# Performance work log

Hardware: AMD Instinct MI355X
Metric: run time of the kernel (lower is better)

## Reference

```python
import jax, jax.numpy as jnp
import numpy as np

N_NODES = 50000
N_EDGES = 800000
N_GRAPHS = 64
D_IN = 768
D_HID = 256


def gcn_conv(x, src, dst, W, b, n_nodes):
    """PyG GCNConv: symmetric-normalized aggregation with self-loops.
    out = D^{-1/2} (A + I) D^{-1/2} (x @ W) + b
    """
    h = x @ W  # [N, C_out]
    # degree from target nodes, counting the implicit self-loop (+1)
    deg = jax.ops.segment_sum(jnp.ones((src.shape[0],), h.dtype), dst,
                              num_segments=n_nodes) + 1.0
    dinv = jax.lax.rsqrt(deg)  # deg >= 1 always (self-loop)
    norm = (dinv[src] * dinv[dst])[:, None]  # [E, 1]
    agg = jax.ops.segment_sum(h[src] * norm, dst, num_segments=n_nodes)
    # self-loop contribution: norm_ii = dinv_i^2
    agg = agg + (dinv * dinv)[:, None] * h
    return agg + b


def global_mean_pool(x, batch, n_graphs):
    s = jax.ops.segment_sum(x, batch, num_segments=n_graphs)
    cnt = jax.ops.segment_sum(jnp.ones((x.shape[0],), x.dtype), batch,
                              num_segments=n_graphs)
    return s / jnp.maximum(cnt, 1.0)[:, None]


def setup_inputs() -> dict:
    key = jax.random.key(0)
    ks = jax.random.split(key, 12)
    x = jax.random.normal(ks[0], (N_NODES, D_IN), jnp.float32)
    edge_index = jax.random.randint(ks[1], (2, N_EDGES), 0, N_NODES, jnp.int64)
    batch = jnp.sort(jax.random.randint(ks[2], (N_NODES,), 0, N_GRAPHS, jnp.int64))
    def glorot(k, shape):
        lim = np.sqrt(6.0 / (shape[0] + shape[1]))
        return jax.random.uniform(k, shape, jnp.float32, -lim, lim)
    return {
        "x": x, "edge_index": edge_index, "batch": batch,
        "W1": glorot(ks[3], (D_IN, D_HID)), "b1": jnp.zeros((D_HID,), jnp.float32),
        "W2": glorot(ks[4], (D_HID, D_HID)), "b2": jnp.zeros((D_HID,), jnp.float32),
        "W3": glorot(ks[5], (D_HID, D_HID)), "b3": jnp.zeros((D_HID,), jnp.float32),
        "Wl": glorot(ks[6], (D_HID, D_IN)), "bl": jnp.zeros((D_IN,), jnp.float32),
    }


def reference(x, edge_index, batch, W1, b1, W2, b2, W3, b3, Wl, bl):
    src, dst = edge_index[0], edge_index[1]
    n = x.shape[0]
    # dropout is identity in eval mode
    h = jax.nn.relu(gcn_conv(x, src, dst, W1, b1, n))
    h = jax.nn.relu(gcn_conv(h, src, dst, W2, b2, n))
    h = gcn_conv(h, src, dst, W3, b3, n)
    g = global_mean_pool(h, batch, N_GRAPHS)  # [G, D_HID]
    return g @ Wl + bl  # [G, D_IN]
```

## Files before the change

kernel.cpp:

```cpp
#include <hip/hip_runtime.h>
#include <hip/hip_bf16.h>

#define D_IN 768
#define D_HID 256

typedef __attribute__((ext_vector_type(8))) short short8;
typedef __attribute__((ext_vector_type(4))) float f32x4;

__device__ inline float b2f(unsigned short u) {
    unsigned x = ((unsigned)u) << 16;
    union { unsigned u; float f; } c; c.u = x; return c.f;
}
__device__ inline unsigned short f2b(float v) {
    __hip_bfloat16 h = __float2bfloat16(v);
    return *(unsigned short*)&h;
}

__device__ inline void gload_lds16(const void* g, void* l) {
    __builtin_amdgcn_global_load_lds(
        (const __attribute__((address_space(1))) unsigned int*)g,
        (__attribute__((address_space(3))) unsigned int*)l, 16, 0, 0);
}


__global__ void k_count(const int* __restrict__ dst, int* __restrict__ deg, int E) {
    int i = blockIdx.x * 256 + threadIdx.x;
    if (i < E) atomicAdd(&deg[dst[i]], 1);
}

__global__ void k_dinv(const int* __restrict__ deg, float* __restrict__ dinv, int N) {
    int i = blockIdx.x * 256 + threadIdx.x;
    if (i < N) dinv[i] = rsqrtf((float)deg[i] + 1.0f);
}

__global__ __launch_bounds__(1024) void k_scan(const int* __restrict__ deg,
                                               int* __restrict__ row_ptr, int N) {
    __shared__ int wsum[16];
    __shared__ int carry_s;
    int t = threadIdx.x;
    int lane = t & 63, wid = t >> 6;
    if (t == 0) carry_s = 0;
    __syncthreads();
    for (int base = 0; base < N; base += 1024) {
        int i = base + t;
        int v = (i < N) ? deg[i] : 0;
        int s = v;
        #pragma unroll
        for (int d = 1; d < 64; d <<= 1) {
            int tmp = __shfl_up(s, d);
            if (lane >= d) s += tmp;
        }
        if (lane == 63) wsum[wid] = s;
        __syncthreads();
        if (wid == 0 && lane < 16) {
            int ws = wsum[lane];
            #pragma unroll
            for (int d = 1; d < 16; d <<= 1) {
                int tmp = __shfl_up(ws, d);
                if (lane >= d) ws += tmp;
            }
            wsum[lane] = ws;
        }
        __syncthreads();
        int carry = carry_s;
        int woff = (wid > 0) ? wsum[wid - 1] : 0;
        if (i < N) row_ptr[i] = carry + woff + s - v;
        __syncthreads();
        if (t == 0) carry_s = carry + wsum[15];
        __syncthreads();
    }
    if (t == 0) row_ptr[N] = carry_s;
}

__global__ void k_fill(const int* __restrict__ src, const int* __restrict__ dst,
                       const int* __restrict__ row_ptr, int* __restrict__ wptr,
                       int* __restrict__ csr_src, int E) {
    int i = blockIdx.x * 256 + threadIdx.x;
    if (i < E) {
        int d = dst[i];
        int w = atomicAdd(&wptr[d], 1);
        csr_src[row_ptr[d] + w] = src[i];
    }
}

__global__ void k_bounds(const int* __restrict__ batch, int* __restrict__ cnt,
                         int* __restrict__ offg, int N, int G) {
    int g = threadIdx.x;
    if (g >= G) return;
    auto lower = [&](int key) {
        int lo = 0, hi = N;
        while (lo < hi) {
            int mid = (lo + hi) >> 1;
            if (batch[mid] < key) lo = mid + 1; else hi = mid;
        }
        return lo;
    };
    int lo = lower(g);
    int hi = lower(g + 1);
    offg[g] = lo;
    cnt[g] = hi - lo;
}

__global__ void k_prep_B(const float* __restrict__ W, short* __restrict__ Bp, int KA) {
    int t = blockIdx.x * 256 + threadIdx.x;
    if (t >= KA * 256) return;
    int k = t >> 8, n = t & 255;
    float v = W[(size_t)k * 256 + n];
    unsigned short h = f2b(v);
    unsigned short l = f2b(v - b2f(h));
    int c = k >> 5, q = (k >> 3) & 3, j = k & 7;
    int tile = n >> 4, ln = n & 15;
    size_t base = (size_t)c * 16384 + (size_t)(tile * 4 + q) * 128 + ln * 8 + j;
    Bp[base] = (short)h;
    Bp[base + 8192] = (short)l;
}

template <int MODE>
__global__ __launch_bounds__(256, 2) void k_gemm4(const void* __restrict__ Av,
                                                  const short* __restrict__ Bp,
                                                  unsigned short* __restrict__ C,
                                                  int M) {
    constexpr int KA = (MODE == 1) ? D_IN : D_HID;
    constexpr int NCH = KA / 32;
    __shared__ short Bs[2][16384];

    int t = threadIdx.x;
    int lane = t & 63, w = t >> 6;
    int ln = lane & 15, q = lane >> 4;
    int bm = blockIdx.x * 64;

    const char* Abase[4];
    #pragma unroll
    for (int s = 0; s < 4; ++s) {
        int rr = bm + s * 16 + ln;
        rr = (rr < M) ? rr : (M - 1);
        Abase[s] = (const char*)Av + (size_t)rr * KA * ((MODE == 1) ? 4 : 2);
    }

    f32x4 acc[4][4];
    #pragma unroll
    for (int s = 0; s < 4; ++s)
        #pragma unroll
        for (int tt = 0; tt < 4; ++tt) acc[s][tt] = (f32x4){0.f, 0.f, 0.f, 0.f};

    auto stage = [&](int c, int pb) {
        #pragma unroll
        for (int i = 0; i < 8; ++i) {
            int seg = i * 4 + w;
            gload_lds16(Bp + (size_t)c * 16384 + seg * 512 + lane * 8,
                        &Bs[pb][seg * 512]);
        }
    };

    stage(0, 0);
    __syncthreads();

    for (int c = 0; c < NCH; ++c) {
        int pb = c & 1;
        if (c + 1 < NCH) stage(c + 1, pb ^ 1);

        short8 a_hi[4], a_lo[4];
        #pragma unroll
        for (int s = 0; s < 4; ++s) {
            if (MODE == 1) {
                const float* Af = (const float*)(Abase[s]) + c * 32 + q * 8;
                f32x4 v0 = *(const f32x4*)Af;
                f32x4 v1 = *(const f32x4*)(Af + 4);
                float vv[8] = {v0[0], v0[1], v0[2], v0[3], v1[0], v1[1], v1[2], v1[3]};
                #pragma unroll
                for (int j = 0; j < 8; ++j) {
                    unsigned short h = f2b(vv[j]);
                    a_hi[s][j] = (short)h;
                    a_lo[s][j] = (short)f2b(vv[j] - b2f(h));
                }
            } else {
                const unsigned short* Ab = (const unsigned short*)(Abase[s]) + c * 32 + q * 8;
                a_hi[s] = *(const short8*)Ab;
            }
        }

        #pragma unroll
        for (int tt = 0; tt < 4; ++tt) {
            int T = w * 4 + tt;
            const short* bp = &Bs[pb][(size_t)(T * 4 + q) * 128 + ln * 8];
            short8 bh = *(const short8*)bp;
            short8 bl = *(const short8*)(bp + 8192);
            #pragma unroll
            for (int s = 0; s < 4; ++s) {
                acc[s][tt] = __builtin_amdgcn_mfma_f32_16x16x32_bf16(a_hi[s], bh, acc[s][tt], 0, 0, 0);
                if (MODE == 1)
                    acc[s][tt] = __builtin_amdgcn_mfma_f32_16x16x32_bf16(a_lo[s], bh, acc[s][tt], 0, 0, 0);
                acc[s][tt] = __builtin_amdgcn_mfma_f32_16x16x32_bf16(
                    (MODE == 1) ? a_hi[s] : a_hi[s], bl, acc[s][tt], 0, 0, 0);
            }
        }
        __syncthreads();
    }

    #pragma unroll
    for (int s = 0; s < 4; ++s)
        #pragma unroll
        for (int tt = 0; tt < 4; ++tt)
            #pragma unroll
            for (int r = 0; r < 4; ++r) {
                int row = bm + s * 16 + q * 4 + r;
                if (row < M)
                    C[(size_t)row * 256 + w * 64 + tt * 16 + ln] = f2b(acc[s][tt][r]);
            }
}

template <int RELU, int OUTBF>
__global__ __launch_bounds__(256) void k_agg(const unsigned short* __restrict__ hin,
                                             void* __restrict__ hout,
                                             const int* __restrict__ row_ptr,
                                             const int* __restrict__ csr_src,
                                             const float* __restrict__ dinv,
                                             const float* __restrict__ bias, int N) {
    int w = threadIdx.x >> 6;
    int lane = threadIdx.x & 63;
    int row = blockIdx.x * 4 + w;
    if (row >= N) return;
    int c4 = lane * 4;
    int s = row_ptr[row], e = row_ptr[row + 1];
    float a0 = 0.f, a1 = 0.f, a2 = 0.f, a3 = 0.f;
    int j = s;
    for (; j + 4 <= e; j += 4) {
        int u0 = csr_src[j], u1 = csr_src[j + 1], u2 = csr_src[j + 2], u3 = csr_src[j + 3];
        float d0 = dinv[u0], d1 = dinv[u1], d2 = dinv[u2], d3 = dinv[u3];
        ushort4 v0 = *(const ushort4*)&hin[(size_t)u0 * 256 + c4];
        ushort4 v1 = *(const ushort4*)&hin[(size_t)u1 * 256 + c4];
        ushort4 v2 = *(const ushort4*)&hin[(size_t)u2 * 256 + c4];
        ushort4 v3 = *(const ushort4*)&hin[(size_t)u3 * 256 + c4];
        a0 += d0 * b2f(v0.x) + d1 * b2f(v1.x) + d2 * b2f(v2.x) + d3 * b2f(v3.x);
        a1 += d0 * b2f(v0.y) + d1 * b2f(v1.y) + d2 * b2f(v2.y) + d3 * b2f(v3.y);
        a2 += d0 * b2f(v0.z) + d1 * b2f(v1.z) + d2 * b2f(v2.z) + d3 * b2f(v3.z);
        a3 += d0 * b2f(v0.w) + d1 * b2f(v1.w) + d2 * b2f(v2.w) + d3 * b2f(v3.w);
    }
    for (; j < e; ++j) {
        int u = csr_src[j];
        float d = dinv[u];
        ushort4 v = *(const ushort4*)&hin[(size_t)u * 256 + c4];
        a0 += d * b2f(v.x); a1 += d * b2f(v.y); a2 += d * b2f(v.z); a3 += d * b2f(v.w);
    }
    float di = dinv[row];
    float dii = di * di;
    ushort4 vs = *(const ushort4*)&hin[(size_t)row * 256 + c4];
    float4 bb = *(const float4*)&bias[c4];
    a0 = a0 * di + dii * b2f(vs.x) + bb.x;
    a1 = a1 * di + dii * b2f(vs.y) + bb.y;
    a2 = a2 * di + dii * b2f(vs.z) + bb.z;
    a3 = a3 * di + dii * b2f(vs.w) + bb.w;
    if (RELU) {
        a0 = fmaxf(a0, 0.f); a1 = fmaxf(a1, 0.f);
        a2 = fmaxf(a2, 0.f); a3 = fmaxf(a3, 0.f);
    }
    if (OUTBF) {
        ushort4 o; o.x = f2b(a0); o.y = f2b(a1); o.z = f2b(a2); o.w = f2b(a3);
        *(ushort4*)((unsigned short*)hout + (size_t)row * 256 + c4) = o;
    } else {
        *(float4*)((float*)hout + (size_t)row * 256 + c4) = make_float4(a0, a1, a2, a3);
    }
}

__global__ __launch_bounds__(256) void k_pool(const float* __restrict__ h,
                                              const int* __restrict__ cnt,
                                              const int* __restrict__ offg,
                                              float* __restrict__ g) {
    int gi = blockIdx.x, slice = blockIdx.y;
    int c = threadIdx.x;
    int start = offg[gi], n = cnt[gi];
    int per = (n + (int)gridDim.y - 1) / (int)gridDim.y;
    int r0 = slice * per;
    int r1 = min(n, r0 + per);
    float acc = 0.f;
    for (int r = r0; r < r1; ++r) acc += h[(size_t)(start + r) * D_HID + c];
    if (r1 > r0) atomicAdd(&g[gi * D_HID + c], acc);
}

__global__ __launch_bounds__(256) void k_final(const float* __restrict__ g,
                                               const int* __restrict__ cnt,
                                               const float* __restrict__ Wl,
                                               const float* __restrict__ bl,
                                               float* __restrict__ out) {
    __shared__ float gs[D_HID];
    int t = threadIdx.x;
    int gi = blockIdx.y;
    int c = blockIdx.x * 256 + t;
    float inv = 1.0f / (float)max(cnt[gi], 1);
    gs[t] = g[gi * D_HID + t] * inv;
    __syncthreads();
    float acc = bl[c];
    #pragma unroll 8
    for (int k = 0; k < D_HID; ++k) acc = fmaf(gs[k], Wl[(size_t)k * D_IN + c], acc);
    out[(size_t)gi * D_IN + c] = acc;
}


extern "C" void kernel_launch(void* const* d_in, const int* in_sizes, int n_in,
                              void* d_out, int out_size, void* d_ws, size_t ws_size,
                              hipStream_t stream) {
    const float* x     = (const float*)d_in[0];
    const int*   ei    = (const int*)d_in[1];
    const int*   batch = (const int*)d_in[2];
    const float* W1 = (const float*)d_in[3];
    const float* b1 = (const float*)d_in[4];
    const float* W2 = (const float*)d_in[5];
    const float* b2 = (const float*)d_in[6];
    const float* W3 = (const float*)d_in[7];
    const float* b3 = (const float*)d_in[8];
    const float* Wl = (const float*)d_in[9];
    const float* bl = (const float*)d_in[10];
    float* out = (float*)d_out;

    int N = in_sizes[2];
    int E = in_sizes[1] / 2;
    int G = out_size / D_IN;
    const int* srcp = ei;
    const int* dstp = ei + E;

    char* ws = (char*)d_ws;
    size_t o = 0;
    auto alloc = [&](size_t bytes) -> char* {
        char* p = ws + o;
        o += (bytes + 255) & ~(size_t)255;
        return p;
    };
    int*   deg     = (int*)alloc((size_t)N * 4);
    int*   wptr    = (int*)alloc((size_t)N * 4);
    int*   row_ptr = (int*)alloc((size_t)(N + 1) * 4);
    int*   cnt     = (int*)alloc((size_t)G * 4);
    int*   offg    = (int*)alloc((size_t)G * 4);
    int*   csr_src = (int*)alloc((size_t)E * 4);
    float* dinv    = (float*)alloc((size_t)N * 4);
    float* gbuf    = (float*)alloc((size_t)G * D_HID * 4);
    unsigned short* hG  = (unsigned short*)alloc((size_t)N * D_HID * 2);
    unsigned short* hA2 = (unsigned short*)alloc((size_t)N * D_HID * 2);
    float* hF      = (float*)alloc((size_t)N * D_HID * 4);
    short* Bp1     = (short*)alloc((size_t)(D_IN / 32) * 16384 * 2);
    short* Bp2     = (short*)alloc((size_t)(D_HID / 32) * 16384 * 2);
    short* Bp3     = (short*)alloc((size_t)(D_HID / 32) * 16384 * 2);

    hipMemsetAsync(deg, 0, (size_t)N * 4, stream);
    hipMemsetAsync(wptr, 0, (size_t)N * 4, stream);
    hipMemsetAsync(gbuf, 0, (size_t)G * D_HID * 4, stream);

    int gE = (E + 255) / 256;
    int gN = (N + 255) / 256;

    k_count<<<gE, 256, 0, stream>>>(dstp, deg, E);
    k_dinv<<<gN, 256, 0, stream>>>(deg, dinv, N);
    k_scan<<<1, 1024, 0, stream>>>(deg, row_ptr, N);
    k_fill<<<gE, 256, 0, stream>>>(srcp, dstp, row_ptr, wptr, csr_src, E);
    k_bounds<<<1, 64, 0, stream>>>(batch, cnt, offg, N, G);

    k_prep_B<<<D_IN, 256, 0, stream>>>(W1, Bp1, D_IN);
    k_prep_B<<<D_HID, 256, 0, stream>>>(W2, Bp2, D_HID);
    k_prep_B<<<D_HID, 256, 0, stream>>>(W3, Bp3, D_HID);

    int gemm_grid = (N + 63) / 64;
    int agg_grid = (N + 3) / 4;

    k_gemm4<1><<<gemm_grid, 256, 0, stream>>>(x, Bp1, hG, N);
    k_agg<1, 1><<<agg_grid, 256, 0, stream>>>(hG, hA2, row_ptr, csr_src, dinv, b1, N);
    k_gemm4<2><<<gemm_grid, 256, 0, stream>>>(hA2, Bp2, hG, N);
    k_agg<1, 1><<<agg_grid, 256, 0, stream>>>(hG, hA2, row_ptr, csr_src, dinv, b2, N);
    k_gemm4<2><<<gemm_grid, 256, 0, stream>>>(hA2, Bp3, hG, N);
    k_agg<0, 0><<<agg_grid, 256, 0, stream>>>(hG, hF, row_ptr, csr_src, dinv, b3, N);

    dim3 pool_grid(G, 8);
    k_pool<<<pool_grid, 256, 0, stream>>>(hF, cnt, offg, gbuf);
    dim3 fin_grid(D_IN / 256, G);
    k_final<<<fin_grid, 256, 0, stream>>>(gbuf, cnt, Wl, bl, out);
}
```

Measured before the change: 786.2 us.

## Load GEMM B fragments directly from global and register-prefetch A tiles

The GEMM kernel no longer stages B (the split hi/lo bf16 weights) into double-buffered LDS with async global-to-LDS loads and per-chunk barriers. Each wave now reads its B fragments straight from global memory, relying on L2/L1 since all blocks share the same small weight matrix. A software prefetch loads the next K-chunk of A into registers while the current chunk's MFMAs run. This removes LDS traffic and __syncthreads, but adds redundant global loads of B per wave and raises register pressure.

```diff
diff --git a/kernel.cpp b/kernel.cpp
--- a/kernel.cpp
+++ b/kernel.cpp
@@ -14,12 +14,6 @@
 __device__ inline unsigned short f2b(float v) {
     __hip_bfloat16 h = __float2bfloat16(v);
     return *(unsigned short*)&h;
-}
-
-__device__ inline void gload_lds16(const void* g, void* l) {
-    __builtin_amdgcn_global_load_lds(
-        (const __attribute__((address_space(1))) unsigned int*)g,
-        (__attribute__((address_space(3))) unsigned int*)l, 16, 0, 0);
 }
 
 
@@ -116,13 +110,12 @@
 }
 
 template <int MODE>
-__global__ __launch_bounds__(256, 2) void k_gemm4(const void* __restrict__ Av,
+__global__ __launch_bounds__(256, 2) void k_gemm5(const void* __restrict__ Av,
                                                   const short* __restrict__ Bp,
                                                   unsigned short* __restrict__ C,
                                                   int M) {
     constexpr int KA = (MODE == 1) ? D_IN : D_HID;
     constexpr int NCH = KA / 32;
-    __shared__ short Bs[2][16384];
 
     int t = threadIdx.x;
     int lane = t & 63, w = t >> 6;
@@ -137,64 +130,89 @@
         Abase[s] = (const char*)Av + (size_t)rr * KA * ((MODE == 1) ? 4 : 2);
     }
 
+    const short* Bl = Bp + (size_t)w * 2048 + q * 128 + ln * 8;
+
     f32x4 acc[4][4];
     #pragma unroll
     for (int s = 0; s < 4; ++s)
         #pragma unroll
         for (int tt = 0; tt < 4; ++tt) acc[s][tt] = (f32x4){0.f, 0.f, 0.f, 0.f};
 
-    auto stage = [&](int c, int pb) {
-        #pragma unroll
-        for (int i = 0; i < 8; ++i) {
-            int seg = i * 4 + w;
-            gload_lds16(Bp + (size_t)c * 16384 + seg * 512 + lane * 8,
-                        &Bs[pb][seg * 512]);
-        }
-    };
-
-    stage(0, 0);
-    __syncthreads();
-
-    for (int c = 0; c < NCH; ++c) {
-        int pb = c & 1;
-        if (c + 1 < NCH) stage(c + 1, pb ^ 1);
-
-        short8 a_hi[4], a_lo[4];
+    if constexpr (MODE == 1) {
+        f32x4 cur0[4], cur1[4], nxt0[4], nxt1[4];
         #pragma unroll
         for (int s = 0; s < 4; ++s) {
-            if (MODE == 1) {
-                const float* Af = (const float*)(Abase[s]) + c * 32 + q * 8;
-                f32x4 v0 = *(const f32x4*)Af;
-                f32x4 v1 = *(const f32x4*)(Af + 4);
-                float vv[8] = {v0[0], v0[1], v0[2], v0[3], v1[0], v1[1], v1[2], v1[3]};
+            const float* Af = (const float*)(Abase[s]) + q * 8;
+            cur0[s] = *(const f32x4*)Af;
+            cur1[s] = *(const f32x4*)(Af + 4);
+        }
+        for (int c = 0; c < NCH; ++c) {
+            if (c + 1 < NCH) {
+                #pragma unroll
+                for (int s = 0; s < 4; ++s) {
+                    const float* Af = (const float*)(Abase[s]) + (c + 1) * 32 + q * 8;
+                    nxt0[s] = *(const f32x4*)Af;
+                    nxt1[s] = *(const f32x4*)(Af + 4);
+                }
+            }
+            const short* bc = Bl + (size_t)c * 16384;
+            short8 bh[4], blo[4];
+            #pragma unroll
+            for (int tt = 0; tt < 4; ++tt) {
+                bh[tt]  = *(const short8*)(bc + tt * 512);
+                blo[tt] = *(const short8*)(bc + tt * 512 + 8192);
+            }
+            short8 a_hi[4], a_lo[4];
+            #pragma unroll
+            for (int s = 0; s < 4; ++s) {
+                float vv[8] = {cur0[s][0], cur0[s][1], cur0[s][2], cur0[s][3],
+                               cur1[s][0], cur1[s][1], cur1[s][2], cur1[s][3]};
                 #pragma unroll
                 for (int j = 0; j < 8; ++j) {
                     unsigned short h = f2b(vv[j]);
                     a_hi[s][j] = (short)h;
                     a_lo[s][j] = (short)f2b(vv[j] - b2f(h));
                 }
-            } else {
-                const unsigned short* Ab = (const unsigned short*)(Abase[s]) + c * 32 + q * 8;
-                a_hi[s] = *(const short8*)Ab;
-            }
-        }
-
-        #pragma unroll
-        for (int tt = 0; tt < 4; ++tt) {
-            int T = w * 4 + tt;
-            const short* bp = &Bs[pb][(size_t)(T * 4 + q) * 128 + ln * 8];
-            short8 bh = *(const short8*)bp;
-            short8 bl = *(const short8*)(bp + 8192);
-            #pragma unroll
-            for (int s = 0; s < 4; ++s) {
-                acc[s][tt] = __builtin_amdgcn_mfma_f32_16x16x32_bf16(a_hi[s], bh, acc[s][tt], 0, 0, 0);
-                if (MODE == 1)
-                    acc[s][tt] = __builtin_amdgcn_mfma_f32_16x16x32_bf16(a_lo[s], bh, acc[s][tt], 0, 0, 0);
-                acc[s][tt] = __builtin_amdgcn_mfma_f32_16x16x32_bf16(
-                    (MODE == 1) ? a_hi[s] : a_hi[s], bl, acc[s][tt], 0, 0, 0);
-            }
-        }
-        __syncthreads();
+            }
+            #pragma unroll
+            for (int tt = 0; tt < 4; ++tt)
+                #pragma unroll
+                for (int s = 0; s < 4; ++s) {
+                    acc[s][tt] = __builtin_amdgcn_mfma_f32_16x16x32_bf16(a_hi[s], bh[tt],  acc[s][tt], 0, 0, 0);
+                    acc[s][tt] = __builtin_amdgcn_mfma_f32_16x16x32_bf16(a_lo[s], bh[tt],  acc[s][tt], 0, 0, 0);
+                    acc[s][tt] = __builtin_amdgcn_mfma_f32_16x16x32_bf16(a_hi[s], blo[tt], acc[s][tt], 0, 0, 0);
+                }
+            #pragma unroll
+            for (int s = 0; s < 4; ++s) { cur0[s] = nxt0[s]; cur1[s] = nxt1[s]; }
+        }
+    } else {
+        short8 cur[4], nxt[4];
+        #pragma unroll
+        for (int s = 0; s < 4; ++s)
+            cur[s] = *(const short8*)((const unsigned short*)(Abase[s]) + q * 8);
+        for (int c = 0; c < NCH; ++c) {
+            if (c + 1 < NCH) {
+                #pragma unroll
+                for (int s = 0; s < 4; ++s)
+                    nxt[s] = *(const short8*)((const unsigned short*)(Abase[s]) + (c + 1) * 32 + q * 8);
+            }
+            const short* bc = Bl + (size_t)c * 16384;
+            short8 bh[4], blo[4];
+            #pragma unroll
+            for (int tt = 0; tt < 4; ++tt) {
+                bh[tt]  = *(const short8*)(bc + tt * 512);
+                blo[tt] = *(const short8*)(bc + tt * 512 + 8192);
+            }
+            #pragma unroll
+            for (int tt = 0; tt < 4; ++tt)
+                #pragma unroll
+                for (int s = 0; s < 4; ++s) {
+                    acc[s][tt] = __builtin_amdgcn_mfma_f32_16x16x32_bf16(cur[s], bh[tt],  acc[s][tt], 0, 0, 0);
+                    acc[s][tt] = __builtin_amdgcn_mfma_f32_16x16x32_bf16(cur[s], blo[tt], acc[s][tt], 0, 0, 0);
+                }
+            #pragma unroll
+            for (int s = 0; s < 4; ++s) cur[s] = nxt[s];
+        }
     }
 
     #pragma unroll
@@ -360,11 +378,11 @@
     int gemm_grid = (N + 63) / 64;
     int agg_grid = (N + 3) / 4;
 
-    k_gemm4<1><<<gemm_grid, 256, 0, stream>>>(x, Bp1, hG, N);
+    k_gemm5<1><<<gemm_grid, 256, 0, stream>>>(x, Bp1, hG, N);
     k_agg<1, 1><<<agg_grid, 256, 0, stream>>>(hG, hA2, row_ptr, csr_src, dinv, b1, N);
-    k_gemm4<2><<<gemm_grid, 256, 0, stream>>>(hA2, Bp2, hG, N);
+    k_gemm5<2><<<gemm_grid, 256, 0, stream>>>(hA2, Bp2, hG, N);
     k_agg<1, 1><<<agg_grid, 256, 0, stream>>>(hG, hA2, row_ptr, csr_src, dinv, b2, N);
-    k_gemm4<2><<<gemm_grid, 256, 0, stream>>>(hA2, Bp3, hG, N);
+    k_gemm5<2><<<gemm_grid, 256, 0, stream>>>(hA2, Bp3, hG, N);
     k_agg<0, 0><<<agg_grid, 256, 0, stream>>>(hG, hF, row_ptr, csr_src, dinv, b3, N);
 
     dim3 pool_grid(G, 8);
```

Measured after the change: 771.3 us. About the same (-1.9%).
